# Kernel optimization log

Hardware: AMD Instinct MI355X
Metric: run time of the kernel (lower is better)

Reference implementation:

```python
import jax, jax.numpy as jnp
import numpy as np

N_BANDS = 5
B = 256
L = 800
T = N_BANDS * L            # concatenated length
N = T - (N_BANDS - 1) - 1  # = 3995; length after dropping pads, minus 1


def setup_inputs() -> dict:
    key = jax.random.key(0)
    k1, k2 = jax.random.split(key)
    # times in [0, 1000): n_bands tensors of [B, L], stacked -> [n_bands, B, L]
    input_times = jax.random.uniform(k1, (N_BANDS, B, L), dtype=jnp.float32) * 1000.0
    N_total = jax.random.randint(k2, (B,), N // 2, N + 1, dtype=jnp.int32)
    N_total = N_total.at[0].set(N)  # ensure max(N_total) == N (static shape)
    return {"input_times": input_times, "N_total": N_total}


def reference(input_times, N_total):
    # sort_times: concat the n_bands [B, L] tensors along axis 1, sort, drop pads
    concat = jnp.transpose(input_times, (1, 0, 2)).reshape(B, T)  # == concat along axis 1
    sorted_times = jnp.sort(concat, axis=1)[:, N_BANDS - 1:]      # [B, N+1]
    st = sorted_times[:, :N + 1]                                  # N = max(N_total) (static)

    # banded delta matrix [N, N+1]: row i has -1 at col i, +1 at col i+1
    delta = jnp.eye(N, N + 1, k=1, dtype=jnp.float32) - jnp.eye(N, N + 1, k=0, dtype=jnp.float32)

    # batched matvec (original tiles delta per batch; broadcasting is equivalent math)
    diffs = jnp.einsum('ij,bj->bi', delta, st)                    # [B, N]

    mask = (jnp.arange(N)[None, :] < N_total[:, None]).astype(jnp.float32)
    return (diffs * mask)[:, :, None]                             # [B, N, 1]
```

## Files before the change

kernel.cpp:

```cpp
#include <hip/hip_runtime.h>
#include <float.h>

#define NB 5
#define BB 256
#define LL 800
#define TT (NB * LL)
#define NN (TT - (NB - 1) - 1)

constexpr int BLOCK = 1024;
constexpr int NBUK  = 4096;
constexpr int EPT   = 4;
constexpr int BPT   = NBUK / BLOCK;

__global__ __launch_bounds__(BLOCK)
void bucket_rank_diff(const float* __restrict__ in,
                      const int* __restrict__ ntotal,
                      float* __restrict__ out)
{
    __shared__ float scat[TT];
    __shared__ float srt[TT];
    __shared__ int   cnt[NBUK];
    __shared__ int   bstart[NBUK];
    __shared__ int   wsum[16];
    __shared__ int   woff[16];

    const int b    = blockIdx.x;
    const int tid  = threadIdx.x;
    const int lane = tid & 63;
    const int wid  = tid >> 6;

    #pragma unroll
    for (int k = 0; k < BPT; ++k) cnt[tid + k * BLOCK] = 0;
    __syncthreads();

    float v[EPT];
    int   bk[EPT];
    int   pp[EPT];
    const float scale = (float)NBUK / 1000.0f;
    #pragma unroll
    for (int k = 0; k < EPT; ++k) {
        int j = tid + k * BLOCK;
        if (j < TT) {
            int band = j / LL;
            int l    = j - band * LL;
            float x  = in[(band * BB + b) * LL + l];
            int bb   = (int)(x * scale);
            bb = bb < 0 ? 0 : (bb > NBUK - 1 ? NBUK - 1 : bb);
            v[k]  = x;
            bk[k] = bb;
            atomicAdd(&cnt[bb], 1);
        } else {
            bk[k] = -1; v[k] = 0.0f;
        }
    }
    __syncthreads();

    int c[BPT];
    int s = 0;
    #pragma unroll
    for (int k = 0; k < BPT; ++k) { c[k] = cnt[BPT * tid + k]; s += c[k]; }
    int inc = s;
    #pragma unroll
    for (int d = 1; d < 64; d <<= 1) {
        int t = __shfl_up(inc, d);
        if (lane >= d) inc += t;
    }
    if (lane == 63) wsum[wid] = inc;
    __syncthreads();
    if (tid < 64) {
        int w  = (tid < 16) ? wsum[tid] : 0;
        int wi = w;
        #pragma unroll
        for (int d = 1; d < 16; d <<= 1) {
            int t = __shfl_up(wi, d);
            if (lane >= d) wi += t;
        }
        if (tid < 16) woff[tid] = wi - w;
    }
    __syncthreads();
    int run = (inc - s) + woff[wid];
    #pragma unroll
    for (int k = 0; k < BPT; ++k) {
        bstart[BPT * tid + k] = run;
        cnt[BPT * tid + k]    = run;
        run += c[k];
    }
    __syncthreads();

    #pragma unroll
    for (int k = 0; k < EPT; ++k) {
        if (bk[k] >= 0) {
            pp[k] = atomicAdd(&cnt[bk[k]], 1);
            scat[pp[k]] = v[k];
        }
    }
    __syncthreads();

    #pragma unroll
    for (int k = 0; k < EPT; ++k) {
        if (bk[k] >= 0) {
            int lo = bstart[bk[k]];
            int hi = cnt[bk[k]];
            float x = v[k];
            int   p = pp[k];
            int   r = lo;
            for (int j = lo; j < hi; ++j) {
                float w = scat[j];
                if (w < x || (w == x && j < p)) ++r;
            }
            srt[r] = x;
        }
    }
    __syncthreads();

    const int nt = ntotal[b];
    #pragma unroll
    for (int k = 0; k < EPT; ++k) {
        int i = tid + k * BLOCK;
        if (i < NN) {
            float d = srt[i + NB] - srt[i + NB - 1];
            out[b * NN + i] = (i < nt) ? d : 0.0f;
        }
    }
}

extern "C" void kernel_launch(void* const* d_in, const int* in_sizes, int n_in,
                              void* d_out, int out_size, void* d_ws, size_t ws_size,
                              hipStream_t stream) {
    const float* in  = (const float*)d_in[0];
    const int*   nt  = (const int*)d_in[1];
    float*       out = (float*)d_out;
    (void)in_sizes; (void)n_in; (void)out_size; (void)d_ws; (void)ws_size;
    bucket_rank_diff<<<BB, BLOCK, 0, stream>>>(in, nt, out);
}
```

Measured before the change: 12.40 us.

## Split each row's sort across four blocks by value range

Each batch row is now handled by four 256-thread blocks instead of one 1024-thread block, and each block owns one quarter of the value range. Every block reads the whole row, counts the elements below its range and keeps their maximum as the left neighbour, then bucket-sorts only its own share into a smaller shared-memory buffer and writes that slice of the diffs. The aim is more blocks in flight and less shared memory per block. In exchange each input element is read four times, and a fixed buffer capacity of 2048 assumes the uniform value distribution.

```diff
diff --git a/kernel.cpp b/kernel.cpp
--- a/kernel.cpp
+++ b/kernel.cpp
@@ -5,55 +5,70 @@
 #define BB 256
 #define LL 800
 #define TT (NB * LL)
-#define NN (TT - (NB - 1) - 1)
+#define NN (TT - NB)
 
-constexpr int BLOCK = 1024;
-constexpr int NBUK  = 4096;
-constexpr int EPT   = 4;
-constexpr int BPT   = NBUK / BLOCK;
+constexpr int BPR  = 4;
+constexpr int THR  = 256;
+constexpr int NBUK = 1024;
+constexpr int GBUK = NBUK * BPR;
+constexpr int EPT  = 16;
+constexpr int BPT  = NBUK / THR;
+constexpr int CAP  = 2048;
 
-__global__ __launch_bounds__(BLOCK)
-void bucket_rank_diff(const float* __restrict__ in,
-                      const int* __restrict__ ntotal,
-                      float* __restrict__ out)
+__global__ __launch_bounds__(THR, 4)
+void range_split_sort_diff(const float* __restrict__ in,
+                           const int* __restrict__ ntotal,
+                           float* __restrict__ out)
 {
-    __shared__ float scat[TT];
-    __shared__ float srt[TT];
+    __shared__ float scat[CAP];
+    __shared__ float srt[CAP];
     __shared__ int   cnt[NBUK];
     __shared__ int   bstart[NBUK];
-    __shared__ int   wsum[16];
-    __shared__ int   woff[16];
+    __shared__ int   wsum[4];
+    __shared__ int   wcb[4];
+    __shared__ float wpm[4];
 
-    const int b    = blockIdx.x;
+    const int blk  = blockIdx.x;
+    const int b    = blk >> 2;
+    const int h    = blk & 3;
     const int tid  = threadIdx.x;
     const int lane = tid & 63;
     const int wid  = tid >> 6;
+    const int gbase = h * NBUK;
 
     #pragma unroll
-    for (int k = 0; k < BPT; ++k) cnt[tid + k * BLOCK] = 0;
+    for (int k = 0; k < BPT; ++k) cnt[tid + k * THR] = 0;
     __syncthreads();
 
     float v[EPT];
-    int   bk[EPT];
-    int   pp[EPT];
-    const float scale = (float)NBUK / 1000.0f;
+    int   myg[EPT];
+    int   cb = 0;
+    float pm = -FLT_MAX;
+    const float scale = (float)GBUK / 1000.0f;
     #pragma unroll
     for (int k = 0; k < EPT; ++k) {
-        int j = tid + k * BLOCK;
+        int j = tid + k * THR;
         if (j < TT) {
             int band = j / LL;
             int l    = j - band * LL;
             float x  = in[(band * BB + b) * LL + l];
-            int bb   = (int)(x * scale);
-            bb = bb < 0 ? 0 : (bb > NBUK - 1 ? NBUK - 1 : bb);
-            v[k]  = x;
-            bk[k] = bb;
-            atomicAdd(&cnt[bb], 1);
-        } else {
-            bk[k] = -1; v[k] = 0.0f;
-        }
+            int g    = (int)(x * scale);
+            g = g < 0 ? 0 : (g > GBUK - 1 ? GBUK - 1 : g);
+            v[k]   = x;
+            myg[k] = g;
+            if (g < gbase) { ++cb; pm = fmaxf(pm, x); }
+            else if ((g >> 10) == h) atomicAdd(&cnt[g & (NBUK - 1)], 1);
+        } else { myg[k] = -1; v[k] = 0.0f; }
     }
+    #pragma unroll
+    for (int d = 1; d < 64; d <<= 1) {
+        cb += __shfl_xor(cb, d);
+        pm  = fmaxf(pm, __shfl_xor(pm, d));
+    }
+    if (lane == 0) { wcb[wid] = cb; wpm[wid] = pm; }
     __syncthreads();
+    const int   below = wcb[0] + wcb[1] + wcb[2] + wcb[3];
+    const float pred  = fmaxf(fmaxf(wpm[0], wpm[1]), fmaxf(wpm[2], wpm[3]));
 
     int c[BPT];
     int s = 0;
@@ -67,58 +82,55 @@
     }
     if (lane == 63) wsum[wid] = inc;
     __syncthreads();
-    if (tid < 64) {
-        int w  = (tid < 16) ? wsum[tid] : 0;
-        int wi = w;
-        #pragma unroll
-        for (int d = 1; d < 16; d <<= 1) {
-            int t = __shfl_up(wi, d);
-            if (lane >= d) wi += t;
-        }
-        if (tid < 16) woff[tid] = wi - w;
-    }
-    __syncthreads();
-    int run = (inc - s) + woff[wid];
+    int wo = 0;
+    #pragma unroll
+    for (int w = 0; w < 4; ++w) if (w < wid) wo += wsum[w];
+    int run = (inc - s) + wo;
     #pragma unroll
     for (int k = 0; k < BPT; ++k) {
         bstart[BPT * tid + k] = run;
         cnt[BPT * tid + k]    = run;
         run += c[k];
     }
+    const int m = wsum[0] + wsum[1] + wsum[2] + wsum[3];
     __syncthreads();
 
+    int pos[EPT];
     #pragma unroll
     for (int k = 0; k < EPT; ++k) {
-        if (bk[k] >= 0) {
-            pp[k] = atomicAdd(&cnt[bk[k]], 1);
-            scat[pp[k]] = v[k];
+        pos[k] = -1;
+        if (myg[k] >= 0 && (myg[k] >> 10) == h) {
+            int p = atomicAdd(&cnt[myg[k] & (NBUK - 1)], 1);
+            if (p < CAP) scat[p] = v[k];
+            pos[k] = p;
         }
     }
     __syncthreads();
 
     #pragma unroll
     for (int k = 0; k < EPT; ++k) {
-        if (bk[k] >= 0) {
-            int lo = bstart[bk[k]];
-            int hi = cnt[bk[k]];
+        if (pos[k] >= 0) {
+            int bkt = myg[k] & (NBUK - 1);
+            int lo  = bstart[bkt];
+            int hi  = cnt[bkt];
             float x = v[k];
-            int   p = pp[k];
+            int   p = pos[k];
             int   r = lo;
             for (int j = lo; j < hi; ++j) {
                 float w = scat[j];
                 if (w < x || (w == x && j < p)) ++r;
             }
-            srt[r] = x;
+            if (r < CAP) srt[r] = x;
         }
     }
     __syncthreads();
 
     const int nt = ntotal[b];
-    #pragma unroll
-    for (int k = 0; k < EPT; ++k) {
-        int i = tid + k * BLOCK;
-        if (i < NN) {
-            float d = srt[i + NB] - srt[i + NB - 1];
+    for (int r = tid; r < m; r += THR) {
+        int i = below + r - NB;
+        if (i >= 0 && i < NN) {
+            float left = (r > 0) ? srt[r - 1] : pred;
+            float d    = srt[r] - left;
             out[b * NN + i] = (i < nt) ? d : 0.0f;
         }
     }
@@ -131,5 +143,5 @@
     const int*   nt  = (const int*)d_in[1];
     float*       out = (float*)d_out;
     (void)in_sizes; (void)n_in; (void)out_size; (void)d_ws; (void)ws_size;
-    bucket_rank_diff<<<BB, BLOCK, 0, stream>>>(in, nt, out);
+    range_split_sort_diff<<<BB * BPR, THR, 0, stream>>>(in, nt, out);
 }
```

Result: slower. 23.87 us (+92.4%).

## Vectorize input loads and reuse histogram atomic offsets for scatter

Applied to the files above, without the earlier changes.

Each thread now loads four contiguous floats with one float4 read instead of four strided scalar reads, so only 1000 of 1024 threads are active. The offset returned by the histogram atomicAdd is kept and added to the bucket start, which removes the second round of shared-memory atomics in the scatter phase. The warp-offset scan becomes a serial sum over 16 wave totals, dropping one barrier, and bucket end positions are read from an extra bstart entry. Each thread now does more serial work per element, and the within-bucket order follows atomic order, which the tie-break on position still handles.

```diff
diff --git a/kernel.cpp b/kernel.cpp
--- a/kernel.cpp
+++ b/kernel.cpp
@@ -5,24 +5,23 @@
 #define BB 256
 #define LL 800
 #define TT (NB * LL)
-#define NN (TT - (NB - 1) - 1)
+#define NN (TT - NB)
 
 constexpr int BLOCK = 1024;
 constexpr int NBUK  = 4096;
-constexpr int EPT   = 4;
 constexpr int BPT   = NBUK / BLOCK;
+constexpr int NV    = TT / 4;
 
 __global__ __launch_bounds__(BLOCK)
-void bucket_rank_diff(const float* __restrict__ in,
-                      const int* __restrict__ ntotal,
-                      float* __restrict__ out)
+void bucket_rank_diff2(const float* __restrict__ in,
+                       const int* __restrict__ ntotal,
+                       float* __restrict__ out)
 {
     __shared__ float scat[TT];
     __shared__ float srt[TT];
     __shared__ int   cnt[NBUK];
-    __shared__ int   bstart[NBUK];
+    __shared__ int   bstart[NBUK + 1];
     __shared__ int   wsum[16];
-    __shared__ int   woff[16];
 
     const int b    = blockIdx.x;
     const int tid  = threadIdx.x;
@@ -33,24 +32,23 @@
     for (int k = 0; k < BPT; ++k) cnt[tid + k * BLOCK] = 0;
     __syncthreads();
 
-    float v[EPT];
-    int   bk[EPT];
-    int   pp[EPT];
-    const float scale = (float)NBUK / 1000.0f;
-    #pragma unroll
-    for (int k = 0; k < EPT; ++k) {
-        int j = tid + k * BLOCK;
-        if (j < TT) {
-            int band = j / LL;
-            int l    = j - band * LL;
-            float x  = in[(band * BB + b) * LL + l];
-            int bb   = (int)(x * scale);
-            bb = bb < 0 ? 0 : (bb > NBUK - 1 ? NBUK - 1 : bb);
-            v[k]  = x;
-            bk[k] = bb;
-            atomicAdd(&cnt[bb], 1);
-        } else {
-            bk[k] = -1; v[k] = 0.0f;
+    float v[4];
+    int   g[4];
+    int   off[4];
+    const bool active = (tid < NV);
+    if (active) {
+        int band = tid / 200;
+        int l4   = tid - band * 200;
+        const float4* p = reinterpret_cast<const float4*>(in + (band * BB + b) * LL) + l4;
+        float4 x4 = *p;
+        v[0] = x4.x; v[1] = x4.y; v[2] = x4.z; v[3] = x4.w;
+        const float scale = (float)NBUK / 1000.0f;
+        #pragma unroll
+        for (int k = 0; k < 4; ++k) {
+            int gg = (int)(v[k] * scale);
+            gg = gg < 0 ? 0 : (gg > NBUK - 1 ? NBUK - 1 : gg);
+            g[k]   = gg;
+            off[k] = atomicAdd(&cnt[gg], 1);
         }
     }
     __syncthreads();
@@ -67,42 +65,32 @@
     }
     if (lane == 63) wsum[wid] = inc;
     __syncthreads();
-    if (tid < 64) {
-        int w  = (tid < 16) ? wsum[tid] : 0;
-        int wi = w;
-        #pragma unroll
-        for (int d = 1; d < 16; d <<= 1) {
-            int t = __shfl_up(wi, d);
-            if (lane >= d) wi += t;
-        }
-        if (tid < 16) woff[tid] = wi - w;
-    }
-    __syncthreads();
-    int run = (inc - s) + woff[wid];
+    int wo = 0;
     #pragma unroll
-    for (int k = 0; k < BPT; ++k) {
-        bstart[BPT * tid + k] = run;
-        cnt[BPT * tid + k]    = run;
-        run += c[k];
-    }
+    for (int w = 0; w < 16; ++w) wo += (w < wid) ? wsum[w] : 0;
+    int run = (inc - s) + wo;
+    #pragma unroll
+    for (int k = 0; k < BPT; ++k) { bstart[BPT * tid + k] = run; run += c[k]; }
+    if (tid == 0) bstart[NBUK] = TT;
     __syncthreads();
 
-    #pragma unroll
-    for (int k = 0; k < EPT; ++k) {
-        if (bk[k] >= 0) {
-            pp[k] = atomicAdd(&cnt[bk[k]], 1);
-            scat[pp[k]] = v[k];
+    int pos[4];
+    if (active) {
+        #pragma unroll
+        for (int k = 0; k < 4; ++k) {
+            pos[k] = bstart[g[k]] + off[k];
+            scat[pos[k]] = v[k];
         }
     }
     __syncthreads();
 
-    #pragma unroll
-    for (int k = 0; k < EPT; ++k) {
-        if (bk[k] >= 0) {
-            int lo = bstart[bk[k]];
-            int hi = cnt[bk[k]];
+    if (active) {
+        #pragma unroll
+        for (int k = 0; k < 4; ++k) {
+            int lo = bstart[g[k]];
+            int hi = bstart[g[k] + 1];
             float x = v[k];
-            int   p = pp[k];
+            int   p = pos[k];
             int   r = lo;
             for (int j = lo; j < hi; ++j) {
                 float w = scat[j];
@@ -115,7 +103,7 @@
 
     const int nt = ntotal[b];
     #pragma unroll
-    for (int k = 0; k < EPT; ++k) {
+    for (int k = 0; k < 4; ++k) {
         int i = tid + k * BLOCK;
         if (i < NN) {
             float d = srt[i + NB] - srt[i + NB - 1];
@@ -131,5 +119,5 @@
     const int*   nt  = (const int*)d_in[1];
     float*       out = (float*)d_out;
     (void)in_sizes; (void)n_in; (void)out_size; (void)d_ws; (void)ws_size;
-    bucket_rank_diff<<<BB, BLOCK, 0, stream>>>(in, nt, out);
+    bucket_rank_diff2<<<BB, BLOCK, 0, stream>>>(in, nt, out);
 }
```

Result: faster. 11.49 us (-7.4%).
